# Performance work log

Measured on AMD Instinct MI355X. Metric: run time of the kernel, lower is better.

The kernel has to match this reference:

```python
import jax, jax.numpy as jnp
import numpy as np

B_SZ, L, D, N = 2, 2048, 1024, 16


def setup_inputs() -> dict:
    key = jax.random.key(0)
    ks = jax.random.split(key, 6)
    x = jax.random.normal(ks[0], (B_SZ, L, D), dtype=jnp.float32)
    W_b = jax.random.normal(ks[1], (N, D), dtype=jnp.float32) * (1.0 / np.sqrt(D))
    W_c = jax.random.normal(ks[2], (N, D), dtype=jnp.float32) * (1.0 / np.sqrt(D))
    # scaled so softplus(s_delta) stays in a sane range (avoids exp overflow)
    W_delta = jax.random.normal(ks[3], (1, D), dtype=jnp.float32) * 0.02
    # negative A (standard for stable SSMs) keeps exp(Delta*A) bounded
    A = -jnp.abs(jax.random.normal(ks[4], (D, N), dtype=jnp.float32))
    delta_param = jax.random.normal(ks[5], (D,), dtype=jnp.float32) * 0.1
    return {"x": x, "W_b": W_b, "W_c": W_c, "W_delta": W_delta, "A": A, "delta_param": delta_param}


def reference(x, W_b, W_c, W_delta, A, delta_param):
    # Input-dependent projections (torch Linear: x @ W.T)
    B = jnp.einsum("bld,nd->bln", x, W_b)                      # [b,l,n]
    C = jnp.einsum("bld,nd->bln", x, W_c)                      # [b,l,n]
    s_delta = jnp.einsum("bld,od->blo", x, W_delta)            # [b,l,1]
    # repeat_interleave(d) of a length-1 axis == broadcast over d
    Delta = jax.nn.softplus(s_delta + delta_param)             # [b,l,d]
    # ZOH discretization
    dA = Delta[..., None] * A                                  # [b,l,d,n]
    A_bar = jnp.exp(dA)                                        # [b,l,d,n]
    B_bar = (A_bar - 1.0) / dA * (Delta[..., None] * B[:, :, None, :])  # [b,l,d,n]
    deltaB_x = B_bar * x[..., None]                            # [b,l,d,n]
    # pack all computed quantities into one array: [b,l,2d+1,n]
    return jnp.concatenate([A_bar, deltaB_x, C[:, :, None, :]], axis=2)
```

## Files before the change

### kernel.cpp

```cpp
#include <hip/hip_runtime.h>
#include <cmath>

#define D_DIM 1024
#define N_DIM 16
#define KTOT  2049
#define WS_STRIDE 36

typedef float v4f __attribute__((ext_vector_type(4)));

__global__ __launch_bounds__(256) void proj_kernel(
    const float* __restrict__ x, const float* __restrict__ W_b,
    const float* __restrict__ W_c, const float* __restrict__ W_delta,
    float* __restrict__ ws, float* __restrict__ out)
{
    const int bl   = blockIdx.x;
    const int tid  = threadIdx.x;
    const int wave = tid >> 6;
    const int lane = tid & 63;

    const float* xrow  = x + (size_t)bl * D_DIM;
    const float* Wbase = (wave < 2) ? W_b : W_c;
    const int rowbase  = (wave & 1) * 8;

    float acc[8] = {0.f,0.f,0.f,0.f,0.f,0.f,0.f,0.f};
    float sd = 0.f;

    #pragma unroll
    for (int i = 0; i < 4; ++i) {
        const int off = (lane + (i << 6)) << 2;
        const v4f xv = *(const v4f*)(xrow + off);
        #pragma unroll
        for (int r = 0; r < 8; ++r) {
            const v4f wv = *(const v4f*)(Wbase + (size_t)(rowbase + r) * D_DIM + off);
            acc[r] = fmaf(xv[0], wv[0], acc[r]);
            acc[r] = fmaf(xv[1], wv[1], acc[r]);
            acc[r] = fmaf(xv[2], wv[2], acc[r]);
            acc[r] = fmaf(xv[3], wv[3], acc[r]);
        }
        if (wave == 0) {
            const v4f wv = *(const v4f*)(W_delta + off);
            sd = fmaf(xv[0], wv[0], sd);
            sd = fmaf(xv[1], wv[1], sd);
            sd = fmaf(xv[2], wv[2], sd);
            sd = fmaf(xv[3], wv[3], sd);
        }
    }

    #pragma unroll
    for (int r = 0; r < 8; ++r) {
        #pragma unroll
        for (int m = 32; m >= 1; m >>= 1)
            acc[r] += __shfl_xor(acc[r], m, 64);
    }
    if (wave == 0) {
        #pragma unroll
        for (int m = 32; m >= 1; m >>= 1)
            sd += __shfl_xor(sd, m, 64);
    }

    if (lane == 0) {
        if (wave < 2) {
            float* dst = ws + (size_t)bl * WS_STRIDE + rowbase;
            #pragma unroll
            for (int r = 0; r < 8; ++r) dst[r] = acc[r];
            if (wave == 0) ws[(size_t)bl * WS_STRIDE + 32] = sd;
        } else {
            float* dst = out + ((size_t)bl * KTOT + 2 * D_DIM) * N_DIM + rowbase;
            #pragma unroll
            for (int r = 0; r < 8; ++r) dst[r] = acc[r];
        }
    }
}

__global__ __launch_bounds__(256) void ssm_kernel(
    const float* __restrict__ x, const float* __restrict__ A,
    const float* __restrict__ delta_param, const float* __restrict__ ws,
    float* __restrict__ out)
{
    const int blk   = blockIdx.x;
    const int bl    = blk >> 4;
    const int chunk = blk & 15;
    const int tid   = threadIdx.x;
    const int n4    = tid & 3;
    const int dloc  = tid >> 2;
    const int d     = (chunk << 6) + dloc;

    const float sd = ws[bl * WS_STRIDE + 32];
    const v4f   Bv = *(const v4f*)(ws + bl * WS_STRIDE + (n4 << 2));
    const float dp = delta_param[d];
    const v4f   Av = *(const v4f*)(A + (size_t)d * N_DIM + (n4 << 2));
    const float xv = x[(size_t)bl * D_DIM + d];

    const float z     = sd + dp;
    const float e     = __expf(-fabsf(z));
    const float Delta = fmaxf(z, 0.0f) + __logf(1.0f + e);
    const float dx    = Delta * xv;

    v4f Abar, dbx;
    #pragma unroll
    for (int i = 0; i < 4; ++i) {
        const float dA = Delta * Av[i];
        const float ab = __expf(dA);
        const float em = ab - 1.0f;
        const float r_big = em * __builtin_amdgcn_rcpf(dA);
        const float r_small =
            fmaf(dA, fmaf(dA, fmaf(dA, fmaf(dA, fmaf(dA,
                1.3888889e-3f,
                8.3333333e-3f),
                4.1666667e-2f),
                1.6666667e-1f),
                0.5f), 1.0f);
        const float ratio = (fabsf(dA) < 0.5f) ? r_small : r_big;
        Abar[i] = ab;
        dbx[i]  = ratio * Bv[i] * dx;
    }

    const size_t base = ((size_t)bl * KTOT + d) * N_DIM + (n4 << 2);
    __builtin_nontemporal_store(Abar, (v4f*)(out + base));
    __builtin_nontemporal_store(dbx,  (v4f*)(out + base + (size_t)D_DIM * N_DIM));
}

extern "C" void kernel_launch(void* const* d_in, const int* in_sizes, int n_in,
                              void* d_out, int out_size, void* d_ws, size_t ws_size,
                              hipStream_t stream)
{
    const float* x           = (const float*)d_in[0];
    const float* W_b         = (const float*)d_in[1];
    const float* W_c         = (const float*)d_in[2];
    const float* W_delta     = (const float*)d_in[3];
    const float* A           = (const float*)d_in[4];
    const float* delta_param = (const float*)d_in[5];
    float* out = (float*)d_out;
    float* ws  = (float*)d_ws;

    const int BL = in_sizes[0] / D_DIM;

    proj_kernel<<<BL, 256, 0, stream>>>(x, W_b, W_c, W_delta, ws, out);
    ssm_kernel<<<BL * 16, 256, 0, stream>>>(x, A, delta_param, ws, out);
}
```

Baseline: 547.6 us.

## Fuse projection and SSM discretization into one kernel with shared-memory staging

```diff
diff --git a/kernel.cpp b/kernel.cpp
--- a/kernel.cpp
+++ b/kernel.cpp
@@ -4,23 +4,32 @@
 #define D_DIM 1024
 #define N_DIM 16
 #define KTOT  2049
-#define WS_STRIDE 36
 
 typedef float v4f __attribute__((ext_vector_type(4)));
 
-__global__ __launch_bounds__(256) void proj_kernel(
+__global__ __launch_bounds__(256) void fused_kernel(
     const float* __restrict__ x, const float* __restrict__ W_b,
     const float* __restrict__ W_c, const float* __restrict__ W_delta,
-    float* __restrict__ ws, float* __restrict__ out)
+    const float* __restrict__ A, const float* __restrict__ delta_param,
+    float* __restrict__ out)
 {
+    __shared__ float xs[D_DIM];
+    __shared__ float Bs[N_DIM];
+    __shared__ float sds;
+
     const int bl   = blockIdx.x;
     const int tid  = threadIdx.x;
     const int wave = tid >> 6;
     const int lane = tid & 63;
 
-    const float* xrow  = x + (size_t)bl * D_DIM;
-    const float* Wbase = (wave < 2) ? W_b : W_c;
-    const int rowbase  = (wave & 1) * 8;
+    {
+        const float* xrow = x + (size_t)bl * D_DIM;
+        *(v4f*)(xs + (tid << 2)) = *(const v4f*)(xrow + (tid << 2));
+    }
+    __syncthreads();
+
+    const float* Wbase  = (wave < 2) ? W_b : W_c;
+    const int   rowbase = (wave & 1) * 8;
 
     float acc[8] = {0.f,0.f,0.f,0.f,0.f,0.f,0.f,0.f};
     float sd = 0.f;
@@ -28,7 +37,7 @@
     #pragma unroll
     for (int i = 0; i < 4; ++i) {
         const int off = (lane + (i << 6)) << 2;
-        const v4f xv = *(const v4f*)(xrow + off);
+        const v4f xv = *(const v4f*)(xs + off);
         #pragma unroll
         for (int r = 0; r < 8; ++r) {
             const v4f wv = *(const v4f*)(Wbase + (size_t)(rowbase + r) * D_DIM + off);
@@ -60,64 +69,57 @@
 
     if (lane == 0) {
         if (wave < 2) {
-            float* dst = ws + (size_t)bl * WS_STRIDE + rowbase;
             #pragma unroll
-            for (int r = 0; r < 8; ++r) dst[r] = acc[r];
-            if (wave == 0) ws[(size_t)bl * WS_STRIDE + 32] = sd;
+            for (int r = 0; r < 8; ++r) Bs[rowbase + r] = acc[r];
+            if (wave == 0) sds = sd;
         } else {
             float* dst = out + ((size_t)bl * KTOT + 2 * D_DIM) * N_DIM + rowbase;
             #pragma unroll
-            for (int r = 0; r < 8; ++r) dst[r] = acc[r];
+            for (int r = 0; r < 8; ++r)
+                __builtin_nontemporal_store(acc[r], dst + r);
         }
     }
-}
+    __syncthreads();
 
-__global__ __launch_bounds__(256) void ssm_kernel(
-    const float* __restrict__ x, const float* __restrict__ A,
-    const float* __restrict__ delta_param, const float* __restrict__ ws,
-    float* __restrict__ out)
-{
-    const int blk   = blockIdx.x;
-    const int bl    = blk >> 4;
-    const int chunk = blk & 15;
-    const int tid   = threadIdx.x;
-    const int n4    = tid & 3;
-    const int dloc  = tid >> 2;
-    const int d     = (chunk << 6) + dloc;
+    const int n4   = tid & 3;
+    const int dloc = tid >> 2;
+    const float sdv = sds;
+    const v4f   Bv  = *(const v4f*)(Bs + (n4 << 2));
 
-    const float sd = ws[bl * WS_STRIDE + 32];
-    const v4f   Bv = *(const v4f*)(ws + bl * WS_STRIDE + (n4 << 2));
-    const float dp = delta_param[d];
-    const v4f   Av = *(const v4f*)(A + (size_t)d * N_DIM + (n4 << 2));
-    const float xv = x[(size_t)bl * D_DIM + d];
+    for (int chunk = 0; chunk < 16; ++chunk) {
+        const int d   = (chunk << 6) + dloc;
+        const float dp = delta_param[d];
+        const v4f   Av = *(const v4f*)(A + (size_t)d * N_DIM + (n4 << 2));
+        const float xv = xs[d];
 
-    const float z     = sd + dp;
-    const float e     = __expf(-fabsf(z));
-    const float Delta = fmaxf(z, 0.0f) + __logf(1.0f + e);
-    const float dx    = Delta * xv;
+        const float z     = sdv + dp;
+        const float e     = __expf(-fabsf(z));
+        const float Delta = fmaxf(z, 0.0f) + __logf(1.0f + e);
+        const float dx    = Delta * xv;
 
-    v4f Abar, dbx;
-    #pragma unroll
-    for (int i = 0; i < 4; ++i) {
-        const float dA = Delta * Av[i];
-        const float ab = __expf(dA);
-        const float em = ab - 1.0f;
-        const float r_big = em * __builtin_amdgcn_rcpf(dA);
-        const float r_small =
-            fmaf(dA, fmaf(dA, fmaf(dA, fmaf(dA, fmaf(dA,
-                1.3888889e-3f,
-                8.3333333e-3f),
-                4.1666667e-2f),
-                1.6666667e-1f),
-                0.5f), 1.0f);
-        const float ratio = (fabsf(dA) < 0.5f) ? r_small : r_big;
-        Abar[i] = ab;
-        dbx[i]  = ratio * Bv[i] * dx;
+        v4f Abar, dbx;
+        #pragma unroll
+        for (int i = 0; i < 4; ++i) {
+            const float dA = Delta * Av[i];
+            const float ab = __expf(dA);
+            const float em = ab - 1.0f;
+            const float r_big = em * __builtin_amdgcn_rcpf(dA);
+            const float r_small =
+                fmaf(dA, fmaf(dA, fmaf(dA, fmaf(dA, fmaf(dA,
+                    1.3888889e-3f,
+                    8.3333333e-3f),
+                    4.1666667e-2f),
+                    1.6666667e-1f),
+                    0.5f), 1.0f);
+            const float ratio = (fabsf(dA) < 0.5f) ? r_small : r_big;
+            Abar[i] = ab;
+            dbx[i]  = ratio * Bv[i] * dx;
+        }
+
+        const size_t base = ((size_t)bl * KTOT + d) * N_DIM + (n4 << 2);
+        __builtin_nontemporal_store(Abar, (v4f*)(out + base));
+        __builtin_nontemporal_store(dbx,  (v4f*)(out + base + (size_t)D_DIM * N_DIM));
     }
-
-    const size_t base = ((size_t)bl * KTOT + d) * N_DIM + (n4 << 2);
-    __builtin_nontemporal_store(Abar, (v4f*)(out + base));
-    __builtin_nontemporal_store(dbx,  (v4f*)(out + base + (size_t)D_DIM * N_DIM));
 }
 
 extern "C" void kernel_launch(void* const* d_in, const int* in_sizes, int n_in,
@@ -131,10 +133,8 @@
     const float* A           = (const float*)d_in[4];
     const float* delta_param = (const float*)d_in[5];
     float* out = (float*)d_out;
-    float* ws  = (float*)d_ws;
 
     const int BL = in_sizes[0] / D_DIM;
 
-    proj_kernel<<<BL, 256, 0, stream>>>(x, W_b, W_c, W_delta, ws, out);
-    ssm_kernel<<<BL * 16, 256, 0, stream>>>(x, A, delta_param, ws, out);
+    fused_kernel<<<BL, 256, 0, stream>>>(x, W_b, W_c, W_delta, A, delta_param, out);
 }
```

After: 552.4 us. About the same (+0.9%).
